# Kernel tuning notes

Measured on AMD Instinct MI355X. Metric: run time of the kernel, lower is better.

## Reference

```python
import jax, jax.numpy as jnp
import numpy as np

B, T, C = 4, 2048, 1024
H, R, S = 16, 256, 64
D = C // H  # head_dim = 64
SCALE = 1.0 / np.sqrt(S).astype(np.float32)


def setup_inputs() -> dict:
    key = jax.random.key(0)
    ks = jax.random.split(key, 6)
    std = 0.02
    return {
        "hidden_states": jax.random.normal(ks[0], (B, T, C), jnp.float32),
        "basis_w": jax.random.normal(ks[1], (R, C), jnp.float32) * std,
        "u_factor": jax.random.normal(ks[2], (H, R, S), jnp.float32) * std,
        "v_factor": jax.random.normal(ks[3], (H, R, S), jnp.float32) * std,
        "v_proj_w": jax.random.normal(ks[4], (C, C), jnp.float32) * std,
        "v_proj_b": jnp.zeros((C,), jnp.float32),
        "o_proj_w": jax.random.normal(ks[5], (C, C), jnp.float32) * std,
        "o_proj_b": jnp.zeros((C,), jnp.float32),
    }


def reference(hidden_states, basis_w, u_factor, v_factor, v_proj_w, v_proj_b,
              o_proj_w, o_proj_b):
    x = hidden_states
    # shared latent basis: [B,T,R]
    latent = jnp.einsum('btc,rc->btr', x, basis_w)
    # head-specific low-rank Q/K: [B,H,T,S]
    q = jnp.einsum('btr,hrs->bhts', latent, u_factor)
    k = jnp.einsum('btr,hrs->bhts', latent, v_factor)
    # V: standard projection, [B,H,T,D]
    v = (jnp.einsum('btc,dc->btd', x, v_proj_w) + v_proj_b)
    v = v.reshape(B, T, H, D).transpose(0, 2, 1, 3)
    # causal attention with full TxT scores (faithful to reference math)
    att = jnp.einsum('bhts,bhus->bhtu', q, k) * SCALE
    causal = jnp.tril(jnp.ones((T, T), bool))
    att = jnp.where(causal, att, -jnp.inf)
    att = jax.nn.softmax(att, axis=-1)
    y = jnp.einsum('bhtu,bhud->bhtd', att, v)
    y = y.transpose(0, 2, 1, 3).reshape(B, T, C)
    y = jnp.einsum('btc,dc->btd', y, o_proj_w) + o_proj_b
    return y
```

## Files before the change

kernel.cpp:

```cpp
#include <hip/hip_runtime.h>
#include <hip/hip_bf16.h>
#include <cstddef>
#include <cstdint>

#define Bn 4
#define Tn 2048
#define Cn 1024
#define Hn 16
#define Rn 256
static constexpr float SCALE = 0.125f;

typedef __attribute__((ext_vector_type(8))) short bf16x8;
typedef __attribute__((ext_vector_type(4))) short bf16x4;
typedef __attribute__((ext_vector_type(4))) float f32x4;

__device__ inline short f2bf(float v) {
  return __builtin_bit_cast(short, __float2bfloat16(v));
}
__device__ inline float bf2f(short s) {
  return __builtin_bit_cast(float, (unsigned)(unsigned short)s << 16);
}
__device__ inline float fexp2(float x) {
  float r;
  asm("v_exp_f32 %0, %1" : "=v"(r) : "v"(x));
  return r;
}

__device__ inline void gld16(const short* g, short* l) {
  __builtin_amdgcn_global_load_lds(
      (const __attribute__((address_space(1))) unsigned*)g,
      (__attribute__((address_space(3))) unsigned*)l, 16, 0, 0);
}

#define NCVT 1343488
__global__ __launch_bounds__(256) void cvtall(
    const float* __restrict__ x, const float* __restrict__ basis,
    const float* __restrict__ vproj, const float* __restrict__ oproj,
    const float* __restrict__ U, const float* __restrict__ V,
    short* __restrict__ dst, short* __restrict__ uvb) {
  int gid = blockIdx.x * 256 + threadIdx.x;
  if (gid < NCVT) {
    const float* src;
    int off;
    if (gid < 1048576) { src = x; off = gid; }
    else if (gid < 1081344) { src = basis; off = gid - 1048576; }
    else if (gid < 1212416) { src = vproj; off = gid - 1081344; }
    else { src = oproj; off = gid - 1212416; }
    const float4* p = (const float4*)src + (size_t)off * 2;
    float4 a = p[0], b = p[1];
    bf16x8 o;
    o[0] = f2bf(a.x); o[1] = f2bf(a.y); o[2] = f2bf(a.z); o[3] = f2bf(a.w);
    o[4] = f2bf(b.x); o[5] = f2bf(b.y); o[6] = f2bf(b.z); o[7] = f2bf(b.w);
    *((bf16x8*)dst + gid) = o;
  } else if (gid < NCVT + 65536) {
    int base = (gid - NCVT) * 8;
    int r0 = base & 255, j = (base >> 8) & 127, h = base >> 15;
    const float QS = 0.18033688f;
    bf16x8 o;
#pragma unroll
    for (int i = 0; i < 8; ++i) {
      int r = r0 + i;
      float v = (j < 64) ? U[((size_t)h * 256 + r) * 64 + j] * QS
                         : V[((size_t)h * 256 + r) * 64 + (j - 64)];
      o[i] = f2bf(v);
    }
    *(bf16x8*)(uvb + base) = o;
  }
}

template <int SMODE, int BIAS>
__global__ __launch_bounds__(256) void gemm_mfma(
    const short* __restrict__ A, const short* __restrict__ Bm,
    const float* __restrict__ bias, void* __restrict__ C0,
    void* __restrict__ C1, int M, int N, int K, int bstride) {
  __shared__ short As[128 * 32];
  __shared__ short Bs[128 * 32];
  const int tid = threadIdx.x;
  const int lane = tid & 63, l16 = lane & 15, quad = lane >> 4;
  const int wave = tid >> 6;
  const int wm = (wave >> 1) * 64, wn = (wave & 1) * 64;
  const int m0 = blockIdx.x * 128, n0 = blockIdx.y * 128;
  const short* Bp = Bm + (size_t)blockIdx.z * bstride;

  f32x4 acc[4][4];
#pragma unroll
  for (int i = 0; i < 4; ++i)
#pragma unroll
    for (int j = 0; j < 4; ++j) acc[i][j] = f32x4{0.f, 0.f, 0.f, 0.f};

  const int arow = tid >> 2, achk = (tid & 3) * 8;
  for (int k0 = 0; k0 < K; k0 += 32) {
#pragma unroll
    for (int p = 0; p < 2; ++p) {
      gld16(A + (size_t)(m0 + p * 64 + arow) * K + k0 + achk,
            As + p * 2048 + tid * 8);
      gld16(Bp + (size_t)(n0 + p * 64 + arow) * K + k0 + achk,
            Bs + p * 2048 + tid * 8);
    }
    __syncthreads();
    bf16x8 af[4], bf[4];
#pragma unroll
    for (int i = 0; i < 4; ++i)
      af[i] = *(const bf16x8*)&As[(wm + i * 16 + l16) * 32 + quad * 8];
#pragma unroll
    for (int j = 0; j < 4; ++j)
      bf[j] = *(const bf16x8*)&Bs[(wn + j * 16 + l16) * 32 + quad * 8];
#pragma unroll
    for (int i = 0; i < 4; ++i)
#pragma unroll
      for (int j = 0; j < 4; ++j)
        acc[i][j] =
            __builtin_amdgcn_mfma_f32_16x16x32_bf16(af[i], bf[j], acc[i][j], 0, 0, 0);
    __syncthreads();
  }

  float bj[4];
#pragma unroll
  for (int j = 0; j < 4; ++j) {
    if (SMODE == 5)
      bj[j] = (n0 >= 256) ? bias[(n0 - 256) + wn + j * 16 + l16] : 0.f;
    else
      bj[j] = BIAS ? bias[n0 + wn + j * 16 + l16] : 0.f;
  }

  if (SMODE == 5 && n0 >= 256) {
    const int h = (n0 + wn - 256) >> 6;
#pragma unroll
    for (int i = 0; i < 4; ++i) {
      int m = m0 + wm + i * 16 + quad * 4;
      int b = m >> 11, t0 = m & 2047;
#pragma unroll
      for (int j = 0; j < 4; ++j) {
        int d = j * 16 + l16;
        bf16x4 pk;
#pragma unroll
        for (int r = 0; r < 4; ++r) pk[r] = f2bf(acc[i][j][r] + bj[j]);
        *(bf16x4*)((short*)C1 + ((size_t)((b * Hn + h) * 64 + d)) * Tn + t0) = pk;
      }
    }
    return;
  }

#pragma unroll
  for (int i = 0; i < 4; ++i) {
#pragma unroll
    for (int r = 0; r < 4; ++r) {
      int m = m0 + wm + i * 16 + quad * 4 + r;
      int b = m >> 11, t = m & 2047;
#pragma unroll
      for (int j = 0; j < 4; ++j) {
        int n = n0 + wn + j * 16 + l16;
        float val = acc[i][j][r] + bj[j];
        if (SMODE == 5) {
          ((short*)C0)[(size_t)m * 256 + n] = f2bf(val);
        } else if (SMODE == 1) {
          int bh = b * Hn + (int)blockIdx.z;
          short* dst = (short*)(n < 64 ? C0 : C1);
          dst[((size_t)bh * Tn + t) * 64 + (n & 63)] = f2bf(val);
        } else {
          ((float*)C0)[(size_t)m * N + n] = val;
        }
      }
    }
  }
}

__constant__ unsigned char ORD6[12] = {12, 30, 31, 26, 27, 8,
                                       22, 23, 18, 19, 4, 0};
#define PP 72
__global__ __launch_bounds__(512) void atn9(
    const short* __restrict__ Qg, const short* __restrict__ Kg,
    const short* __restrict__ VTg, short* __restrict__ Yb,
    short* __restrict__ Opart, float* __restrict__ Lpart) {
  __shared__ short Ks[2][64 * 64];
  __shared__ short Vt[2][64 * 64];
  __shared__ short Ps[8 * 16 * PP];

  const int tid = threadIdx.x;
  const int wave = tid >> 6, lane = tid & 63;
  const int l16 = lane & 15, quad = lane >> 4;
  const unsigned v = ORD6[blockIdx.y];
  const int qt = v >> 2, split = (v >> 1) & 1, half = v & 1;
  const int bh = blockIdx.x;
  const int wtrow = qt * 256 + wave * 32;
  const size_t kb = (size_t)bh * Tn * 64;
  const size_t vb = (size_t)bh * 64 * Tn;
  const int j0 = split ? half * (2 * qt + 2) : 0;
  const int jn = split ? (2 * qt + 2) : (4 * qt + 4);

  bf16x8 qf[2][2];
#pragma unroll
  for (int rg = 0; rg < 2; ++rg)
#pragma unroll
    for (int s = 0; s < 2; ++s)
      qf[rg][s] = *(const bf16x8*)(Qg + kb +
          (size_t)(wtrow + rg * 16 + l16) * 64 + s * 32 + quad * 8);

  f32x4 o[2][4];
#pragma unroll
  for (int rg = 0; rg < 2; ++rg)
#pragma unroll
    for (int dt = 0; dt < 4; ++dt) o[rg][dt] = f32x4{0.f, 0.f, 0.f, 0.f};
  float lp[2][4] = {{0.f, 0.f, 0.f, 0.f}, {0.f, 0.f, 0.f, 0.f}};

  const int srow = tid >> 3;
  const int sseg = (tid & 7) ^ (srow & 7);
#define STAGE7(buf, j)                                                        \
  {                                                                           \
    gld16(Kg + kb + (size_t)((j) * 64 + srow) * 64 + sseg * 8,                \
          &Ks[buf][tid * 8]);                                                 \
    gld16(VTg + vb + (size_t)srow * Tn + (j) * 64 + sseg * 8,                 \
          &Vt[buf][tid * 8]);                                                 \
  }

  STAGE7(0, j0);
  short* pw = &Ps[wave * 16 * PP];
  const int xs = l16 & 7;

  for (int jj = 0; jj < jn; ++jj) {
    const int j = j0 + jj;
    const int cb = jj & 1;
    __syncthreads();
    if (jj + 1 < jn) STAGE7(cb ^ 1, j + 1);

    const bool act1 = (j * 64 <= wtrow + 31);
    const bool act0 = (j * 64 <= wtrow + 15);
    if (!act1) continue;

    f32x4 sa[2][4];
    __builtin_amdgcn_s_setprio(1);
#pragma unroll
    for (int ct = 0; ct < 4; ++ct) {
      bf16x8 k0 = *(const bf16x8*)&Ks[cb][(ct * 16 + l16) * 64 + ((0 + quad) ^ xs) * 8];
      bf16x8 k1 = *(const bf16x8*)&Ks[cb][(ct * 16 + l16) * 64 + ((4 + quad) ^ xs) * 8];
#pragma unroll
      for (int rg = 0; rg < 2; ++rg) {
        if (rg == 0 && !act0) continue;
        f32x4 t = f32x4{0.f, 0.f, 0.f, 0.f};
        t = __builtin_amdgcn_mfma_f32_16x16x32_bf16(k0, qf[rg][0], t, 0, 0, 0);
        t = __builtin_amdgcn_mfma_f32_16x16x32_bf16(k1, qf[rg][1], t, 0, 0, 0);
        sa[rg][ct] = t;
      }
    }
    __builtin_amdgcn_s_setprio(0);

#pragma unroll
    for (int rg = 0; rg < 2; ++rg) {
      if (rg == 0 && !act0) continue;
      const int rbase = wtrow + rg * 16;
      const int trow = rbase + l16;
      const bool full = (j * 64 + 63 <= rbase);
#pragma unroll
      for (int ct = 0; ct < 4; ++ct) {
        const int ubase = j * 64 + ct * 16 + quad * 4;
        bf16x4 pk;
#pragma unroll
        for (int r = 0; r < 4; ++r) {
          float e;
          if (full) {
            e = fexp2(sa[rg][ct][r]);
          } else {
            e = (ubase + r <= trow) ? fexp2(sa[rg][ct][r]) : 0.f;
          }
          lp[rg][r] += e;
          pk[r] = f2bf(e);
        }
        *(bf16x4*)&pw[l16 * PP + ct * 16 + quad * 4] = pk;
      }
      bf16x8 pf0 = *(const bf16x8*)&pw[l16 * PP + quad * 8];
      bf16x8 pf1 = *(const bf16x8*)&pw[l16 * PP + 32 + quad * 8];
      __builtin_amdgcn_s_setprio(1);
#pragma unroll
      for (int dt = 0; dt < 4; ++dt) {
        bf16x8 v0 = *(const bf16x8*)&Vt[cb][(dt * 16 + l16) * 64 + ((0 + quad) ^ xs) * 8];
        bf16x8 v1 = *(const bf16x8*)&Vt[cb][(dt * 16 + l16) * 64 + ((4 + quad) ^ xs) * 8];
        o[rg][dt] = __builtin_amdgcn_mfma_f32_16x16x32_bf16(pf0, v0, o[rg][dt], 0, 0, 0);
        o[rg][dt] = __builtin_amdgcn_mfma_f32_16x16x32_bf16(pf1, v1, o[rg][dt], 0, 0, 0);
      }
      __builtin_amdgcn_s_setprio(0);
    }
  }

  const int row = lane >> 2, cseg = lane & 3;
  if (!split) {
    const int b = bh >> 4, h = bh & 15;
#pragma unroll
    for (int rg = 0; rg < 2; ++rg) {
      float lfull = (lp[rg][0] + lp[rg][1]) + (lp[rg][2] + lp[rg][3]);
      lfull += __shfl_xor(lfull, 16);
      lfull += __shfl_xor(lfull, 32);
      float invf = 1.f / lfull;
      float inv[4];
#pragma unroll
      for (int r = 0; r < 4; ++r) inv[r] = __shfl(invf, quad * 4 + r);
#pragma unroll
      for (int dt = 0; dt < 4; ++dt)
#pragma unroll
        for (int r = 0; r < 4; ++r)
          pw[(quad * 4 + r) * PP + dt * 16 + l16] = f2bf(o[rg][dt][r] * inv[r]);
      bf16x8 y0 = *(const bf16x8*)&pw[row * PP + cseg * 16];
      bf16x8 y1 = *(const bf16x8*)&pw[row * PP + cseg * 16 + 8];
      short* dst = Yb + ((size_t)(b * Tn + wtrow + rg * 16 + row)) * Cn +
                   h * 64 + cseg * 16;
      *(bf16x8*)dst = y0;
      *(bf16x8*)(dst + 8) = y1;
    }
  } else {
    const int slot = (bh * 4 + (qt - 4)) * 2 + half;
#pragma unroll
    for (int rg = 0; rg < 2; ++rg) {
      float lfull = (lp[rg][0] + lp[rg][1]) + (lp[rg][2] + lp[rg][3]);
      lfull += __shfl_xor(lfull, 16);
      lfull += __shfl_xor(lfull, 32);
#pragma unroll
      for (int dt = 0; dt < 4; ++dt)
#pragma unroll
        for (int r = 0; r < 4; ++r)
          pw[(quad * 4 + r) * PP + dt * 16 + l16] = f2bf(o[rg][dt][r]);
      bf16x8 y0 = *(const bf16x8*)&pw[row * PP + cseg * 16];
      bf16x8 y1 = *(const bf16x8*)&pw[row * PP + cseg * 16 + 8];
      const int rrow = wave * 32 + rg * 16 + row;
      short* dst = Opart + ((size_t)slot * 256 + rrow) * 64 + cseg * 16;
      *(bf16x8*)dst = y0;
      *(bf16x8*)(dst + 8) = y1;
      if (quad == 0) Lpart[slot * 256 + wave * 32 + rg * 16 + l16] = lfull;
    }
  }
}

__global__ __launch_bounds__(256) void combine_k(
    const short* __restrict__ Opart, const float* __restrict__ Lpart,
    short* __restrict__ Yb) {
  int gid = blockIdx.x * 256 + threadIdx.x;
  int seg = gid & 7, row = (gid >> 3) & 255, qtr = (gid >> 11) & 3,
      bh = gid >> 13;
  int slotA = (bh * 4 + qtr) * 2, slotB = slotA + 1;
  float la = Lpart[slotA * 256 + row], lb = Lpart[slotB * 256 + row];
  float inv = 1.f / (la + lb);
  bf16x8 a = *(const bf16x8*)(Opart + ((size_t)slotA * 256 + row) * 64 + seg * 8);
  bf16x8 b = *(const bf16x8*)(Opart + ((size_t)slotB * 256 + row) * 64 + seg * 8);
  bf16x8 y;
#pragma unroll
  for (int i = 0; i < 8; ++i) y[i] = f2bf((bf2f(a[i]) + bf2f(b[i])) * inv);
  int t = (qtr + 4) * 256 + row, bb = bh >> 4, h = bh & 15;
  *(bf16x8*)(Yb + ((size_t)(bb * Tn + t)) * Cn + h * 64 + seg * 8) = y;
}

extern "C" void kernel_launch(void* const* d_in, const int* in_sizes, int n_in,
                              void* d_out, int out_size, void* d_ws,
                              size_t ws_size, hipStream_t stream) {
  const float* x        = (const float*)d_in[0];
  const float* basis_w  = (const float*)d_in[1];
  const float* u_factor = (const float*)d_in[2];
  const float* v_factor = (const float*)d_in[3];
  const float* v_proj_w = (const float*)d_in[4];
  const float* v_proj_b = (const float*)d_in[5];
  const float* o_proj_w = (const float*)d_in[6];
  const float* o_proj_b = (const float*)d_in[7];
  float* out = (float*)d_out;

  char* ws = (char*)d_ws;
  const size_t NX = (size_t)Bn * Tn * Cn;
  short* xb      = (short*)ws; ws += NX * 2;
  short* bwb     = (short*)ws; ws += (size_t)Rn * Cn * 2;
  short* vpb     = (short*)ws; ws += (size_t)Cn * Cn * 2;
  short* opb     = (short*)ws; ws += (size_t)Cn * Cn * 2;
  short* uvb     = (short*)ws; ws += (size_t)Hn * 128 * Rn * 2;
  short* latentb = (short*)ws; ws += (size_t)Bn * Tn * Rn * 2;
  short* Qb      = (short*)ws; ws += NX * 2;
  short* Kb      = (short*)ws; ws += NX * 2;
  short* VTb     = (short*)ws; ws += NX * 2;
  short* yb      = (short*)ws; ws += NX * 2;
  short* Opart   = (short*)ws; ws += (size_t)512 * 256 * 64 * 2;
  float* Lpart   = (float*)ws;
  (void)vpb;

  dim3 blk(256);
  cvtall<<<dim3(5504), blk, 0, stream>>>(x, basis_w, v_proj_w, o_proj_w,
                                         u_factor, v_factor, xb, uvb);

  gemm_mfma<5, 1><<<dim3(64, 10, 1), blk, 0, stream>>>(
      xb, bwb, v_proj_b, latentb, VTb, 8192, 1280, 1024, 0);
  gemm_mfma<1, 0><<<dim3(64, 1, 16), blk, 0, stream>>>(
      latentb, uvb, nullptr, Qb, Kb, 8192, 128, 256, 128 * 256);
  atn9<<<dim3(64, 12), dim3(512), 0, stream>>>(Qb, Kb, VTb, yb, Opart, Lpart);
  combine_k<<<dim3(2048), blk, 0, stream>>>(Opart, Lpart, yb);
  gemm_mfma<3, 1><<<dim3(64, 8, 1), blk, 0, stream>>>(
      yb, opb, o_proj_b, out, nullptr, 8192, 1024, 1024, 0);
}
```

Baseline: 275.8 us.

## Split attention loop barrier so V tile loads overlap QK compute

```diff
diff --git a/kernel.cpp b/kernel.cpp
--- a/kernel.cpp
+++ b/kernel.cpp
@@ -168,7 +168,7 @@
 __constant__ unsigned char ORD6[12] = {12, 30, 31, 26, 27, 8,
                                        22, 23, 18, 19, 4, 0};
 #define PP 72
-__global__ __launch_bounds__(512) void atn9(
+__global__ __launch_bounds__(512) void atn11(
     const short* __restrict__ Qg, const short* __restrict__ Kg,
     const short* __restrict__ VTg, short* __restrict__ Yb,
     short* __restrict__ Opart, float* __restrict__ Lpart) {
@@ -195,6 +195,7 @@
     for (int s = 0; s < 2; ++s)
       qf[rg][s] = *(const bf16x8*)(Qg + kb +
           (size_t)(wtrow + rg * 16 + l16) * 64 + s * 32 + quad * 8);
+  asm volatile("" :: "v"(qf[0][0]), "v"(qf[0][1]), "v"(qf[1][0]), "v"(qf[1][1]));
 
   f32x4 o[2][4];
 #pragma unroll
@@ -220,62 +221,81 @@
   for (int jj = 0; jj < jn; ++jj) {
     const int j = j0 + jj;
     const int cb = jj & 1;
-    __syncthreads();
-    if (jj + 1 < jn) STAGE7(cb ^ 1, j + 1);
+    const bool more = (jj + 1 < jn);
+
+    asm volatile("s_waitcnt vmcnt(1)" ::: "memory");
+    __builtin_amdgcn_s_barrier();
+    if (more) STAGE7(cb ^ 1, j + 1);
 
     const bool act1 = (j * 64 <= wtrow + 31);
     const bool act0 = (j * 64 <= wtrow + 15);
-    if (!act1) continue;
-
-    f32x4 sa[2][4];
-    __builtin_amdgcn_s_setprio(1);
-#pragma unroll
-    for (int ct = 0; ct < 4; ++ct) {
-      bf16x8 k0 = *(const bf16x8*)&Ks[cb][(ct * 16 + l16) * 64 + ((0 + quad) ^ xs) * 8];
-      bf16x8 k1 = *(const bf16x8*)&Ks[cb][(ct * 16 + l16) * 64 + ((4 + quad) ^ xs) * 8];
+
+    bf16x8 pf[2][2];
+    if (act1) {
+      f32x4 sa[2][4];
+      __builtin_amdgcn_s_setprio(1);
+#pragma unroll
+      for (int ct = 0; ct < 4; ++ct) {
+        bf16x8 k0 = *(const bf16x8*)&Ks[cb][(ct * 16 + l16) * 64 + ((0 + quad) ^ xs) * 8];
+        bf16x8 k1 = *(const bf16x8*)&Ks[cb][(ct * 16 + l16) * 64 + ((4 + quad) ^ xs) * 8];
+#pragma unroll
+        for (int rg = 0; rg < 2; ++rg) {
+          if (rg == 0 && !act0) continue;
+          f32x4 t = f32x4{0.f, 0.f, 0.f, 0.f};
+          t = __builtin_amdgcn_mfma_f32_16x16x32_bf16(k0, qf[rg][0], t, 0, 0, 0);
+          t = __builtin_amdgcn_mfma_f32_16x16x32_bf16(k1, qf[rg][1], t, 0, 0, 0);
+          sa[rg][ct] = t;
+        }
+      }
+      __builtin_amdgcn_s_setprio(0);
+
 #pragma unroll
       for (int rg = 0; rg < 2; ++rg) {
         if (rg == 0 && !act0) continue;
-        f32x4 t = f32x4{0.f, 0.f, 0.f, 0.f};
-        t = __builtin_amdgcn_mfma_f32_16x16x32_bf16(k0, qf[rg][0], t, 0, 0, 0);
-        t = __builtin_amdgcn_mfma_f32_16x16x32_bf16(k1, qf[rg][1], t, 0, 0, 0);
-        sa[rg][ct] = t;
+        const int rbase = wtrow + rg * 16;
+        const int trow = rbase + l16;
+        const bool full = (j * 64 + 63 <= rbase);
+#pragma unroll
+        for (int ct = 0; ct < 4; ++ct) {
+          const int ubase = j * 64 + ct * 16 + quad * 4;
+          bf16x4 pk;
+#pragma unroll
+          for (int r = 0; r < 4; ++r) {
+            float e;
+            if (full) {
+              e = fexp2(sa[rg][ct][r]);
+            } else {
+              e = (ubase + r <= trow) ? fexp2(sa[rg][ct][r]) : 0.f;
+            }
+            lp[rg][r] += e;
+            pk[r] = f2bf(e);
+          }
+          *(bf16x4*)&pw[l16 * PP + ct * 16 + quad * 4] = pk;
+        }
+        pf[rg][0] = *(const bf16x8*)&pw[l16 * PP + quad * 8];
+        pf[rg][1] = *(const bf16x8*)&pw[l16 * PP + 32 + quad * 8];
       }
     }
-    __builtin_amdgcn_s_setprio(0);
-
-#pragma unroll
-    for (int rg = 0; rg < 2; ++rg) {
-      if (rg == 0 && !act0) continue;
-      const int rbase = wtrow + rg * 16;
-      const int trow = rbase + l16;
-      const bool full = (j * 64 + 63 <= rbase);
-#pragma unroll
-      for (int ct = 0; ct < 4; ++ct) {
-        const int ubase = j * 64 + ct * 16 + quad * 4;
-        bf16x4 pk;
-#pragma unroll
-        for (int r = 0; r < 4; ++r) {
-          float e;
-          if (full) {
-            e = fexp2(sa[rg][ct][r]);
-          } else {
-            e = (ubase + r <= trow) ? fexp2(sa[rg][ct][r]) : 0.f;
-          }
-          lp[rg][r] += e;
-          pk[r] = f2bf(e);
-        }
-        *(bf16x4*)&pw[l16 * PP + ct * 16 + quad * 4] = pk;
-      }
-      bf16x8 pf0 = *(const bf16x8*)&pw[l16 * PP + quad * 8];
-      bf16x8 pf1 = *(const bf16x8*)&pw[l16 * PP + 32 + quad * 8];
+
+    if (more) {
+      asm volatile("s_waitcnt vmcnt(2)" ::: "memory");
+    } else {
+      asm volatile("s_waitcnt vmcnt(0)" ::: "memory");
+    }
+    __builtin_amdgcn_s_barrier();
+
+    if (act1) {
       __builtin_amdgcn_s_setprio(1);
 #pragma unroll
       for (int dt = 0; dt < 4; ++dt) {
         bf16x8 v0 = *(const bf16x8*)&Vt[cb][(dt * 16 + l16) * 64 + ((0 + quad) ^ xs) * 8];
         bf16x8 v1 = *(const bf16x8*)&Vt[cb][(dt * 16 + l16) * 64 + ((4 + quad) ^ xs) * 8];
-        o[rg][dt] = __builtin_amdgcn_mfma_f32_16x16x32_bf16(pf0, v0, o[rg][dt], 0, 0, 0);
-        o[rg][dt] = __builtin_amdgcn_mfma_f32_16x16x32_bf16(pf1, v1, o[rg][dt], 0, 0, 0);
+#pragma unroll
+        for (int rg = 0; rg < 2; ++rg) {
+          if (rg == 0 && !act0) continue;
+          o[rg][dt] = __builtin_amdgcn_mfma_f32_16x16x32_bf16(pf[rg][0], v0, o[rg][dt], 0, 0, 0);
+          o[rg][dt] = __builtin_amdgcn_mfma_f32_16x16x32_bf16(pf[rg][1], v1, o[rg][dt], 0, 0, 0);
+        }
       }
       __builtin_amdgcn_s_setprio(0);
     }
@@ -383,7 +403,7 @@
       xb, bwb, v_proj_b, latentb, VTb, 8192, 1280, 1024, 0);
   gemm_mfma<1, 0><<<dim3(64, 1, 16), blk, 0, stream>>>(
       latentb, uvb, nullptr, Qb, Kb, 8192, 128, 256, 128 * 256);
-  atn9<<<dim3(64, 12), dim3(512), 0, stream>>>(Qb, Kb, VTb, yb, Opart, Lpart);
+  atn11<<<dim3(64, 12), dim3(512), 0, stream>>>(Qb, Kb, VTb, yb, Opart, Lpart);
   combine_k<<<dim3(2048), blk, 0, stream>>>(Opart, Lpart, yb);
   gemm_mfma<3, 1><<<dim3(64, 8, 1), blk, 0, stream>>>(
       yb, opb, o_proj_b, out, nullptr, 8192, 1024, 1024, 0);
```

Result: no change. 279.8 us (+1.5%).

## Load V fragments directly from global memory and remap GEMM blocks across XCDs

Applied to the files above, without the earlier changes.

```diff
diff --git a/kernel.cpp b/kernel.cpp
--- a/kernel.cpp
+++ b/kernel.cpp
@@ -79,7 +79,19 @@
   const int lane = tid & 63, l16 = lane & 15, quad = lane >> 4;
   const int wave = tid >> 6;
   const int wm = (wave >> 1) * 64, wn = (wave & 1) * 64;
-  const int m0 = blockIdx.x * 128, n0 = blockIdx.y * 128;
+
+  int bx = blockIdx.x, by = blockIdx.y;
+  if (SMODE == 3 || SMODE == 5) {
+    int nwg = gridDim.x * gridDim.y;
+    int orig = by * gridDim.x + bx;
+    int qq = nwg >> 3, rr = nwg & 7;
+    int xcd = orig & 7, idx = orig >> 3;
+    int base = xcd < rr ? xcd * (qq + 1) : rr * (qq + 1) + (xcd - rr) * qq;
+    int wg = base + idx;
+    bx = wg % gridDim.x;
+    by = wg / gridDim.x;
+  }
+  const int m0 = bx * 128, n0 = by * 128;
   const short* Bp = Bm + (size_t)blockIdx.z * bstride;
 
   f32x4 acc[4][4];
@@ -168,12 +180,11 @@
 __constant__ unsigned char ORD6[12] = {12, 30, 31, 26, 27, 8,
                                        22, 23, 18, 19, 4, 0};
 #define PP 72
-__global__ __launch_bounds__(512) void atn9(
+__global__ __launch_bounds__(512) void atn12(
     const short* __restrict__ Qg, const short* __restrict__ Kg,
     const short* __restrict__ VTg, short* __restrict__ Yb,
     short* __restrict__ Opart, float* __restrict__ Lpart) {
   __shared__ short Ks[2][64 * 64];
-  __shared__ short Vt[2][64 * 64];
   __shared__ short Ps[8 * 16 * PP];
 
   const int tid = threadIdx.x;
@@ -201,27 +212,24 @@
   for (int rg = 0; rg < 2; ++rg)
 #pragma unroll
     for (int dt = 0; dt < 4; ++dt) o[rg][dt] = f32x4{0.f, 0.f, 0.f, 0.f};
-  float lp[2][4] = {{0.f, 0.f, 0.f, 0.f}, {0.f, 0.f, 0.f, 0.f}};
+  float lp[2] = {0.f, 0.f};
 
   const int srow = tid >> 3;
   const int sseg = (tid & 7) ^ (srow & 7);
-#define STAGE7(buf, j)                                                        \
-  {                                                                           \
-    gld16(Kg + kb + (size_t)((j) * 64 + srow) * 64 + sseg * 8,                \
-          &Ks[buf][tid * 8]);                                                 \
-    gld16(VTg + vb + (size_t)srow * Tn + (j) * 64 + sseg * 8,                 \
-          &Vt[buf][tid * 8]);                                                 \
-  }
-
-  STAGE7(0, j0);
+#define STAGEK(buf, j)                                                        \
+  gld16(Kg + kb + (size_t)((j) * 64 + srow) * 64 + sseg * 8,                  \
+        &Ks[buf][tid * 8]);
+
+  STAGEK(0, j0);
   short* pw = &Ps[wave * 16 * PP];
   const int xs = l16 & 7;
+  const short* Vbase = VTg + vb + (size_t)l16 * Tn + quad * 8;
 
   for (int jj = 0; jj < jn; ++jj) {
     const int j = j0 + jj;
     const int cb = jj & 1;
     __syncthreads();
-    if (jj + 1 < jn) STAGE7(cb ^ 1, j + 1);
+    if (jj + 1 < jn) STAGEK(cb ^ 1, j + 1);
 
     const bool act1 = (j * 64 <= wtrow + 31);
     const bool act0 = (j * 64 <= wtrow + 15);
@@ -254,17 +262,19 @@
       for (int ct = 0; ct < 4; ++ct) {
         const int ubase = j * 64 + ct * 16 + quad * 4;
         bf16x4 pk;
+        float e[4];
 #pragma unroll
         for (int r = 0; r < 4; ++r) {
-          float e;
+          float ev;
           if (full) {
-            e = fexp2(sa[rg][ct][r]);
+            ev = fexp2(sa[rg][ct][r]);
           } else {
-            e = (ubase + r <= trow) ? fexp2(sa[rg][ct][r]) : 0.f;
+            ev = (ubase + r <= trow) ? fexp2(sa[rg][ct][r]) : 0.f;
           }
-          lp[rg][r] += e;
-          pk[r] = f2bf(e);
+          e[r] = ev;
+          pk[r] = f2bf(ev);
         }
+        lp[rg] += (e[0] + e[1]) + (e[2] + e[3]);
         *(bf16x4*)&pw[l16 * PP + ct * 16 + quad * 4] = pk;
       }
       bf16x8 pf0 = *(const bf16x8*)&pw[l16 * PP + quad * 8];
@@ -272,8 +282,9 @@
       __builtin_amdgcn_s_setprio(1);
 #pragma unroll
       for (int dt = 0; dt < 4; ++dt) {
-        bf16x8 v0 = *(const bf16x8*)&Vt[cb][(dt * 16 + l16) * 64 + ((0 + quad) ^ xs) * 8];
-        bf16x8 v1 = *(const bf16x8*)&Vt[cb][(dt * 16 + l16) * 64 + ((4 + quad) ^ xs) * 8];
+        const short* vp = Vbase + (size_t)(dt * 16) * Tn + j * 64;
+        bf16x8 v0 = *(const bf16x8*)vp;
+        bf16x8 v1 = *(const bf16x8*)(vp + 32);
         o[rg][dt] = __builtin_amdgcn_mfma_f32_16x16x32_bf16(pf0, v0, o[rg][dt], 0, 0, 0);
         o[rg][dt] = __builtin_amdgcn_mfma_f32_16x16x32_bf16(pf1, v1, o[rg][dt], 0, 0, 0);
       }
@@ -286,7 +297,7 @@
     const int b = bh >> 4, h = bh & 15;
 #pragma unroll
     for (int rg = 0; rg < 2; ++rg) {
-      float lfull = (lp[rg][0] + lp[rg][1]) + (lp[rg][2] + lp[rg][3]);
+      float lfull = lp[rg];
       lfull += __shfl_xor(lfull, 16);
       lfull += __shfl_xor(lfull, 32);
       float invf = 1.f / lfull;
@@ -309,7 +320,7 @@
     const int slot = (bh * 4 + (qt - 4)) * 2 + half;
 #pragma unroll
     for (int rg = 0; rg < 2; ++rg) {
-      float lfull = (lp[rg][0] + lp[rg][1]) + (lp[rg][2] + lp[rg][3]);
+      float lfull = lp[rg];
       lfull += __shfl_xor(lfull, 16);
       lfull += __shfl_xor(lfull, 32);
 #pragma unroll
@@ -342,7 +353,7 @@
   bf16x8 y;
 #pragma unroll
   for (int i = 0; i < 8; ++i) y[i] = f2bf((bf2f(a[i]) + bf2f(b[i])) * inv);
-  int t = (qtr + 4) * 256 + row, bb = bh >> 4, h = bh & 15;
+  int t = (qtr + 4) * 256 + row, bb = gid >> 17, h = (gid >> 13) & 15;
   *(bf16x8*)(Yb + ((size_t)(bb * Tn + t)) * Cn + h * 64 + seg * 8) = y;
 }
 
@@ -383,7 +394,7 @@
       xb, bwb, v_proj_b, latentb, VTb, 8192, 1280, 1024, 0);
   gemm_mfma<1, 0><<<dim3(64, 1, 16), blk, 0, stream>>>(
       latentb, uvb, nullptr, Qb, Kb, 8192, 128, 256, 128 * 256);
-  atn9<<<dim3(64, 12), dim3(512), 0, stream>>>(Qb, Kb, VTb, yb, Opart, Lpart);
+  atn12<<<dim3(64, 12), dim3(512), 0, stream>>>(Qb, Kb, VTb, yb, Opart, Lpart);
   combine_k<<<dim3(2048), blk, 0, stream>>>(Opart, Lpart, yb);
   gemm_mfma<3, 1><<<dim3(64, 8, 1), blk, 0, stream>>>(
       yb, opb, o_proj_b, out, nullptr, 8192, 1024, 1024, 0);
```

Measured after the change: 378.2 us. 1.37x slower.
